# Optimization experiments

Measured on AMD Instinct MI355X. Metric: run time of the kernel, lower is better.

Reference implementation:

```python
import jax, jax.numpy as jnp
import numpy as np

N_HEADS = 32
N_KV_HEADS = 8
HEAD_DIM = 64
ROPE_THETA = 10000.0
NEG_INF = -1e9


def apply_rope(t, offset=0):
    # t: [B, H, L, hd]; half-split (rotate-half) RoPE convention
    B, H, L, hd = t.shape
    pos = jnp.arange(offset, offset + L, dtype=jnp.float32)            # [L]
    inv_freq = 1.0 / (ROPE_THETA ** (jnp.arange(0, hd, 2, dtype=jnp.float32) / hd))  # [hd/2]
    ang = pos[:, None] * inv_freq[None, :]                              # [L, hd/2]
    cos = jnp.cos(ang).astype(t.dtype)
    sin = jnp.sin(ang).astype(t.dtype)
    t1, t2 = jnp.split(t, 2, axis=-1)                                   # each [B,H,L,hd/2]
    return jnp.concatenate([t1 * cos - t2 * sin, t1 * sin + t2 * cos], axis=-1)


def setup_inputs() -> dict:
    key = jax.random.key(0)
    ks = jax.random.split(key, 6)
    B, L, D = 1, 2048, 2048
    x = jax.random.normal(ks[0], (B, L, D), dtype=jnp.float32)
    attn_scale = jnp.ones((1,), dtype=jnp.float32)
    # causal additive mask: 0 on/below diagonal, -1e9 above
    mask = jnp.where(jnp.tril(jnp.ones((L, L), dtype=bool)), 0.0, NEG_INF).astype(jnp.float32)
    s = 0.02
    Wq = jax.random.normal(ks[1], (N_HEADS * HEAD_DIM, D), dtype=jnp.float32) * s
    Wk = jax.random.normal(ks[2], (N_KV_HEADS * HEAD_DIM, D), dtype=jnp.float32) * s
    Wv = jax.random.normal(ks[3], (N_KV_HEADS * HEAD_DIM, D), dtype=jnp.float32) * s
    Wo = jax.random.normal(ks[4], (D, N_HEADS * HEAD_DIM), dtype=jnp.float32) * s
    return {"x": x, "attn_scale": attn_scale, "mask": mask,
            "Wq": Wq, "Wk": Wk, "Wv": Wv, "Wo": Wo}


def reference(x, attn_scale, mask, Wq, Wk, Wv, Wo):
    B, L, D = x.shape
    scale = HEAD_DIM ** -0.5
    # projections (nn.Linear: y = x @ W.T)
    q = (x @ Wq.T).reshape(B, L, N_HEADS, HEAD_DIM).transpose(0, 2, 1, 3)     # [B,H,L,hd]
    k = (x @ Wk.T).reshape(B, L, N_KV_HEADS, HEAD_DIM).transpose(0, 2, 1, 3)  # [B,Hk,L,hd]
    v = (x @ Wv.T).reshape(B, L, N_KV_HEADS, HEAD_DIM).transpose(0, 2, 1, 3)
    q = apply_rope(q)
    k = apply_rope(k)
    q = q * attn_scale  # elementwise attn_scale applied to queries
    # GQA: repeat kv heads
    rep = N_HEADS // N_KV_HEADS
    k = jnp.repeat(k, rep, axis=1)
    v = jnp.repeat(v, rep, axis=1)
    scores = jnp.einsum('bhld,bhmd->bhlm', q, k) * scale + mask
    probs = jax.nn.softmax(scores, axis=-1)
    out = jnp.einsum('bhlm,bhmd->bhld', probs, v)          # [B,H,L,hd]
    out = out.transpose(0, 2, 1, 3).reshape(B, L, N_HEADS * HEAD_DIM)
    return out @ Wo.T
```

## Files before the change

kernel.cpp:

```cpp
#include <hip/hip_runtime.h>
#include <stdint.h>

typedef short bf16x8 __attribute__((ext_vector_type(8)));
typedef float f32x4 __attribute__((ext_vector_type(4)));

__device__ __forceinline__ unsigned short f2bf(float f) {
  uint32_t u = __float_as_uint(f);
  u = (u + 0x7FFFu + ((u >> 16) & 1u)) >> 16;
  return (unsigned short)u;
}
__device__ __forceinline__ float bf2f(unsigned short h) {
  return __uint_as_float(((uint32_t)h) << 16);
}

__device__ __forceinline__ void gload16(const void* g, void* lds) {
  const __attribute__((address_space(1))) char* gp =
      (const __attribute__((address_space(1))) char*)(uintptr_t)g;
  __attribute__((address_space(3))) char* sp =
      (__attribute__((address_space(3))) char*)(uint32_t)(uintptr_t)lds;
  __builtin_amdgcn_global_load_lds(gp, sp, 16, 0, 0);
}

__global__ void k_cvt_all(const float* __restrict__ x, const float* __restrict__ Wq,
                          const float* __restrict__ Wk, const float* __restrict__ Wv,
                          const float* __restrict__ Wo, unsigned short* __restrict__ xb,
                          unsigned short* __restrict__ Wcat, unsigned short* __restrict__ Wob) {
  int b = blockIdx.x;
  const float* src;
  unsigned short* dst;
  int off;
  if (b < 4096)       { src = x;  dst = xb;                  off = b; }
  else if (b < 8192)  { src = Wq; dst = Wcat;                off = b - 4096; }
  else if (b < 9216)  { src = Wk; dst = Wcat + 2048 * 2048;  off = b - 8192; }
  else if (b < 10240) { src = Wv; dst = Wcat + 2560 * 2048;  off = b - 9216; }
  else                { src = Wo; dst = Wob;                  off = b - 10240; }
  int i = off * 256 + threadIdx.x;
  float4 v = ((const float4*)src)[i];
  ushort4 o;
  o.x = f2bf(v.x); o.y = f2bf(v.y); o.z = f2bf(v.z); o.w = f2bf(v.w);
  ((ushort4*)dst)[i] = o;
}

template <int OUTF32>
__global__ __launch_bounds__(256) void k_gemm(const unsigned short* __restrict__ A,
                                              const unsigned short* __restrict__ B,
                                              void* __restrict__ Cout,
                                              int M, int N, int K) {
  __shared__ unsigned short As[128 * 64];
  __shared__ unsigned short Bs[128 * 64];
  const int tid = threadIdx.x;
  const int w = tid >> 6, lane = tid & 63;
  const int g = lane >> 4, cl = lane & 15;
  const int nTn = N >> 7;
  const int per = gridDim.x >> 3;
  const int bid = (blockIdx.x & 7) * per + (blockIdx.x >> 3);
  const int tm = bid / nTn, tn = bid % nTn;
  const int m0 = tm << 7, n0 = tn << 7;
  const int wm = (w >> 1) << 6, wn = (w & 1) << 6;
  f32x4 acc[4][4] = {};
  for (int kt = 0; kt < K; kt += 64) {
    if (kt) __syncthreads();
#pragma unroll
    for (int it = 0; it < 8; ++it) {
      int cc = tid + it * 256;
      int half = cc >> 10;
      int c3 = cc & 1023;
      int row = c3 >> 3, kb = (c3 & 7) << 4;
      const unsigned short* base = half ? (B + (size_t)(n0 + row) * K + kt)
                                        : (A + (size_t)(m0 + row) * K + kt);
      const char* src = (const char*)base + (kb ^ ((row & 7) << 4));
      char* dstl = (char*)(half ? Bs : As) + c3 * 16;
      gload16(src, dstl);
    }
    asm volatile("s_waitcnt vmcnt(0)" ::: "memory");
    __syncthreads();
#pragma unroll
    for (int ks = 0; ks < 2; ++ks) {
      bf16x8 af[4], bfr[4];
#pragma unroll
      for (int i = 0; i < 4; ++i) {
        int row = wm + i * 16 + cl;
        int kb = ((g << 4) + (ks << 6)) ^ ((row & 7) << 4);
        af[i] = *(const bf16x8*)((const char*)As + row * 128 + kb);
      }
#pragma unroll
      for (int j = 0; j < 4; ++j) {
        int row = wn + j * 16 + cl;
        int kb = ((g << 4) + (ks << 6)) ^ ((row & 7) << 4);
        bfr[j] = *(const bf16x8*)((const char*)Bs + row * 128 + kb);
      }
#pragma unroll
      for (int i = 0; i < 4; ++i)
#pragma unroll
        for (int j = 0; j < 4; ++j)
          acc[i][j] = __builtin_amdgcn_mfma_f32_16x16x32_bf16(af[i], bfr[j], acc[i][j], 0, 0, 0);
    }
  }
#pragma unroll
  for (int i = 0; i < 4; ++i)
#pragma unroll
    for (int j = 0; j < 4; ++j)
#pragma unroll
      for (int r = 0; r < 4; ++r) {
        int row = m0 + wm + i * 16 + (g << 2) + r;
        int col = n0 + wn + j * 16 + cl;
        float v = acc[i][j][r];
        if (OUTF32)
          ((float*)Cout)[(size_t)row * N + col] = v;
        else
          ((unsigned short*)Cout)[(size_t)row * N + col] = f2bf(v);
      }
}

__global__ void k_ropevt(unsigned short* __restrict__ qkv, const float* __restrict__ scale_p,
                         unsigned short* __restrict__ vt) {
  __shared__ unsigned short tl[64][80];
  if (blockIdx.x < 2560) {
    int idx = blockIdx.x * 256 + threadIdx.x;
    int l = idx / 320;
    int u = idx - l * 320;
    int h = u >> 3;
    int i4 = (u & 7) << 2;
    int colbase = (h < 32) ? (h << 6) : (2048 + ((h - 32) << 6));
    unsigned short* p = qkv + (size_t)l * 3072 + colbase + i4;
    float sc = (h < 32) ? (scale_p[0] * 0.125f * 1.4426950408889634f) : 1.0f;
    ushort4 a = *(const ushort4*)p;
    ushort4 b = *(const ushort4*)(p + 32);
    unsigned short av[4] = {a.x, a.y, a.z, a.w};
    unsigned short bv[4] = {b.x, b.y, b.z, b.w};
    unsigned short r1[4], r2[4];
#pragma unroll
    for (int j = 0; j < 4; ++j) {
      int i = i4 + j;
      float invf = __expf(-(float)i * 0.2878231366242557f);
      float ang = (float)l * invf;
      float cs = cosf(ang), sn = sinf(ang);
      float x1 = bf2f(av[j]), x2 = bf2f(bv[j]);
      r1[j] = f2bf((x1 * cs - x2 * sn) * sc);
      r2[j] = f2bf((x1 * sn + x2 * cs) * sc);
    }
    ushort4 oa = {r1[0], r1[1], r1[2], r1[3]};
    ushort4 ob = {r2[0], r2[1], r2[2], r2[3]};
    *(ushort4*)p = oa;
    *(ushort4*)(p + 32) = ob;
  } else {
    const int tid = threadIdx.x;
    const int bb = blockIdx.x - 2560;
    const int hk = bb >> 5, lt = bb & 31;
    const int l0 = lt << 6;
#pragma unroll
    for (int it = 0; it < 2; ++it) {
      int cc = tid + it * 256;
      int lr = cc >> 3, d0 = (cc & 7) << 3;
      uint4 v = *(const uint4*)(qkv + (size_t)(l0 + lr) * 3072 + 2560 + hk * 64 + d0);
      *(uint4*)&tl[lr][d0] = v;
    }
    __syncthreads();
#pragma unroll
    for (int it = 0; it < 2; ++it) {
      int cc = tid + it * 256;
      int dr = cc >> 3, le = (cc & 7) << 3;
      unsigned short tmp[8] __attribute__((aligned(16)));
#pragma unroll
      for (int j = 0; j < 8; ++j) tmp[j] = tl[le + j][dr];
      *(uint4*)(vt + (size_t)(hk * 64 + dr) * 2048 + l0 + le) = *(const uint4*)tmp;
    }
  }
}

__global__ __launch_bounds__(256) void k_attn(const unsigned short* __restrict__ qkv,
                                              const unsigned short* __restrict__ vt,
                                              unsigned short* __restrict__ ao) {
  __shared__ unsigned short Ks[2][64 * 64];
  __shared__ unsigned short Vs[3][64 * 64];
  __shared__ unsigned short Ps[4 * 16 * 64];
  const int tid = threadIdx.x;
  const int w = tid >> 6, lane = tid & 63;
  const int g = lane >> 4, cl = lane & 15;
  const int h = blockIdx.x & 31;
  const int qb = 31 - (blockIdx.x >> 5);
  const int q0 = qb << 6;
  const int hk = h >> 2;
  const int qg = q0 + w * 16 + cl;

  const unsigned short* qptr = qkv + (size_t)qg * 3072 + h * 64 + g * 8;
  bf16x8 qf0 = *(const bf16x8*)qptr;
  bf16x8 qf1 = *(const bf16x8*)(qptr + 32);

  float m_run = -3e38f, l_run = 0.0f;
  f32x4 acc[4] = {};

  const unsigned short* kbase = qkv + 2048 + hk * 64;
  const unsigned short* vbase = vt + (size_t)hk * 64 * 2048;
  char* myP = (char*)Ps + w * 2048;

  auto stageK = [&](int ck, int b) {
    const int kv0 = ck << 6;
#pragma unroll
    for (int it = 0; it < 2; ++it) {
      int cc = tid + it * 256;
      int row = cc >> 3, kb = (cc & 7) << 4;
      const char* src = (const char*)(kbase + (size_t)(kv0 + row) * 3072) + (kb ^ ((row & 7) << 4));
      gload16(src, (char*)Ks[b] + cc * 16);
    }
  };
  auto stageV = [&](int ck, int b) {
    const int kv0 = ck << 6;
#pragma unroll
    for (int it = 0; it < 2; ++it) {
      int cc = tid + it * 256;
      int row = cc >> 3, kb = (cc & 7) << 4;
      const char* src = (const char*)(vbase + (size_t)row * 2048 + kv0) + (kb ^ ((row & 7) << 4));
      gload16(src, (char*)Vs[b] + cc * 16);
    }
  };

  stageK(0, 0); stageV(0, 0);
  if (qb >= 1) { stageK(1, 1); stageV(1, 1); }
  asm volatile("s_waitcnt vmcnt(0)" ::: "memory");
  __syncthreads();

  float svP[4][4];
  {
    const char* Kc = (const char*)Ks[0];
    __builtin_amdgcn_s_setprio(1);
#pragma unroll
    for (int t = 0; t < 4; ++t) {
      f32x4 st = {};
#pragma unroll
      for (int ks = 0; ks < 2; ++ks) {
        int row = t * 16 + cl;
        int kb = ((g << 4) + (ks << 6)) ^ ((row & 7) << 4);
        bf16x8 kf = *(const bf16x8*)(Kc + row * 128 + kb);
        st = __builtin_amdgcn_mfma_f32_16x16x32_bf16(kf, ks ? qf1 : qf0, st, 0, 0, 0);
      }
#pragma unroll
      for (int r = 0; r < 4; ++r) svP[t][r] = st[r];
    }
    __builtin_amdgcn_s_setprio(0);
  }
  __syncthreads();

  for (int i = 0; i <= qb; ++i) {
    if (i + 2 <= qb) { stageK(i + 2, (i + 2) & 1); stageV(i + 2, (i + 2) % 3); }

    float svN[4][4];
    if (i < qb) {
      const char* Kc = (const char*)Ks[(i + 1) & 1];
      __builtin_amdgcn_s_setprio(1);
#pragma unroll
      for (int t = 0; t < 4; ++t) {
        f32x4 st = {};
#pragma unroll
        for (int ks = 0; ks < 2; ++ks) {
          int row = t * 16 + cl;
          int kb = ((g << 4) + (ks << 6)) ^ ((row & 7) << 4);
          bf16x8 kf = *(const bf16x8*)(Kc + row * 128 + kb);
          st = __builtin_amdgcn_mfma_f32_16x16x32_bf16(kf, ks ? qf1 : qf0, st, 0, 0, 0);
        }
#pragma unroll
        for (int r = 0; r < 4; ++r) svN[t][r] = st[r];
      }
      __builtin_amdgcn_s_setprio(0);
    }

    if (i == qb) {
      const int kv0 = i << 6;
#pragma unroll
      for (int t = 0; t < 4; ++t)
#pragma unroll
        for (int r = 0; r < 4; ++r) {
          int kvg = kv0 + t * 16 + (g << 2) + r;
          if (kvg > qg) svP[t][r] = -1e9f;
        }
    }
    float pmax = -3e38f;
#pragma unroll
    for (int t = 0; t < 4; ++t)
      pmax = fmaxf(pmax, fmaxf(fmaxf(svP[t][0], svP[t][1]), fmaxf(svP[t][2], svP[t][3])));
    pmax = fmaxf(pmax, __shfl_xor(pmax, 16));
    pmax = fmaxf(pmax, __shfl_xor(pmax, 32));
    if (!__all(pmax - m_run <= 8.0f)) {
      float m_new = fmaxf(m_run, pmax);
      float fac = __builtin_exp2f(m_run - m_new);
      float fr[4];
#pragma unroll
      for (int r = 0; r < 4; ++r) fr[r] = __shfl(fac, (g << 2) + r);
#pragma unroll
      for (int t = 0; t < 4; ++t) {
        acc[t][0] *= fr[0]; acc[t][1] *= fr[1]; acc[t][2] *= fr[2]; acc[t][3] *= fr[3];
      }
      l_run *= fac;
      m_run = m_new;
    }
    float psum = 0.0f;
#pragma unroll
    for (int t = 0; t < 4; ++t) {
      float e0 = __builtin_exp2f(svP[t][0] - m_run);
      float e1 = __builtin_exp2f(svP[t][1] - m_run);
      float e2 = __builtin_exp2f(svP[t][2] - m_run);
      float e3 = __builtin_exp2f(svP[t][3] - m_run);
      psum += (e0 + e1) + (e2 + e3);
      uint32_t d0, d1;
      asm("v_cvt_pk_bf16_f32 %0, %1, %2" : "=v"(d0) : "v"(e0), "v"(e1));
      asm("v_cvt_pk_bf16_f32 %0, %1, %2" : "=v"(d1) : "v"(e2), "v"(e3));
      uint2 dd; dd.x = d0; dd.y = d1;
      int kb = ((t << 5) + (g << 3)) ^ ((cl & 7) << 4);
      *(uint2*)(myP + cl * 128 + kb) = dd;
    }
    psum += __shfl_xor(psum, 16);
    psum += __shfl_xor(psum, 32);
    l_run += psum;

    {
      const char* Vc = (const char*)Vs[i % 3];
      __builtin_amdgcn_s_setprio(1);
#pragma unroll
      for (int ks = 0; ks < 2; ++ks) {
        int kbp = ((g << 4) + (ks << 6)) ^ ((cl & 7) << 4);
        bf16x8 pf = *(const bf16x8*)(myP + cl * 128 + kbp);
#pragma unroll
        for (int t = 0; t < 4; ++t) {
          int row = t * 16 + cl;
          int kbv = ((g << 4) + (ks << 6)) ^ ((row & 7) << 4);
          bf16x8 vf = *(const bf16x8*)(Vc + row * 128 + kbv);
          acc[t] = __builtin_amdgcn_mfma_f32_16x16x32_bf16(pf, vf, acc[t], 0, 0, 0);
        }
      }
      __builtin_amdgcn_s_setprio(0);
    }

    if (i < qb) {
      asm volatile("s_waitcnt vmcnt(0)" ::: "memory");
      __syncthreads();
#pragma unroll
      for (int t = 0; t < 4; ++t)
#pragma unroll
        for (int r = 0; r < 4; ++r) svP[t][r] = svN[t][r];
    }
  }

  float li[4];
#pragma unroll
  for (int r = 0; r < 4; ++r) li[r] = 1.0f / __shfl(l_run, (g << 2) + r);
#pragma unroll
  for (int t = 0; t < 4; ++t)
#pragma unroll
    for (int r = 0; r < 4; ++r) {
      int row = q0 + w * 16 + (g << 2) + r;
      int col = h * 64 + t * 16 + cl;
      ao[(size_t)row * 2048 + col] = f2bf(acc[t][r] * li[r]);
    }
}

extern "C" void kernel_launch(void* const* d_in, const int* in_sizes, int n_in,
                              void* d_out, int out_size, void* d_ws, size_t ws_size,
                              hipStream_t stream) {
  (void)in_sizes; (void)n_in; (void)out_size; (void)ws_size;
  const float* x  = (const float*)d_in[0];
  const float* sc = (const float*)d_in[1];
  const float* Wq = (const float*)d_in[3];
  const float* Wk = (const float*)d_in[4];
  const float* Wv = (const float*)d_in[5];
  const float* Wo = (const float*)d_in[6];
  float* out = (float*)d_out;
  char* ws = (char*)d_ws;
  unsigned short* xb   = (unsigned short*)(ws);
  unsigned short* Wcat = (unsigned short*)(ws + 8388608);
  unsigned short* Wob  = (unsigned short*)(ws + 20971520);
  unsigned short* QKV  = (unsigned short*)(ws + 29360128);
  unsigned short* VT   = (unsigned short*)(ws + 41943040);
  unsigned short* AO   = (unsigned short*)(ws + 44040192);

  k_cvt_all<<<14336, 256, 0, stream>>>(x, Wq, Wk, Wv, Wo, xb, Wcat, Wob);
  k_gemm<0><<<384, 256, 0, stream>>>(xb, Wcat, QKV, 2048, 3072, 2048);
  k_ropevt<<<2816, 256, 0, stream>>>(QKV, sc, VT);
  k_attn<<<1024, 256, 0, stream>>>(QKV, VT, AO);
  k_gemm<1><<<256, 256, 0, stream>>>(AO, Wob, out, 2048, 2048, 2048);
}
```

Baseline: 141.3 us.

## Double-buffer GEMM LDS tiles and loosen attention prefetch waits

```diff
diff --git a/kernel.cpp b/kernel.cpp
--- a/kernel.cpp
+++ b/kernel.cpp
@@ -46,8 +46,8 @@
                                               const unsigned short* __restrict__ B,
                                               void* __restrict__ Cout,
                                               int M, int N, int K) {
-  __shared__ unsigned short As[128 * 64];
-  __shared__ unsigned short Bs[128 * 64];
+  __shared__ unsigned short As[2][128 * 64];
+  __shared__ unsigned short Bs[2][128 * 64];
   const int tid = threadIdx.x;
   const int w = tid >> 6, lane = tid & 63;
   const int g = lane >> 4, cl = lane & 15;
@@ -58,8 +58,8 @@
   const int m0 = tm << 7, n0 = tn << 7;
   const int wm = (w >> 1) << 6, wn = (w & 1) << 6;
   f32x4 acc[4][4] = {};
-  for (int kt = 0; kt < K; kt += 64) {
-    if (kt) __syncthreads();
+
+  auto stage = [&](int kt, int b) {
 #pragma unroll
     for (int it = 0; it < 8; ++it) {
       int cc = tid + it * 256;
@@ -69,11 +69,18 @@
       const unsigned short* base = half ? (B + (size_t)(n0 + row) * K + kt)
                                         : (A + (size_t)(m0 + row) * K + kt);
       const char* src = (const char*)base + (kb ^ ((row & 7) << 4));
-      char* dstl = (char*)(half ? Bs : As) + c3 * 16;
+      char* dstl = (char*)(half ? Bs[b] : As[b]) + c3 * 16;
       gload16(src, dstl);
     }
-    asm volatile("s_waitcnt vmcnt(0)" ::: "memory");
-    __syncthreads();
+  };
+
+  stage(0, 0);
+  asm volatile("s_waitcnt vmcnt(0)" ::: "memory");
+  __syncthreads();
+  int buf = 0;
+
+  for (int kt = 0; kt < K; kt += 64) {
+    if (kt + 64 < K) stage(kt + 64, buf ^ 1);
 #pragma unroll
     for (int ks = 0; ks < 2; ++ks) {
       bf16x8 af[4], bfr[4];
@@ -81,13 +88,13 @@
       for (int i = 0; i < 4; ++i) {
         int row = wm + i * 16 + cl;
         int kb = ((g << 4) + (ks << 6)) ^ ((row & 7) << 4);
-        af[i] = *(const bf16x8*)((const char*)As + row * 128 + kb);
+        af[i] = *(const bf16x8*)((const char*)As[buf] + row * 128 + kb);
       }
 #pragma unroll
       for (int j = 0; j < 4; ++j) {
         int row = wn + j * 16 + cl;
         int kb = ((g << 4) + (ks << 6)) ^ ((row & 7) << 4);
-        bfr[j] = *(const bf16x8*)((const char*)Bs + row * 128 + kb);
+        bfr[j] = *(const bf16x8*)((const char*)Bs[buf] + row * 128 + kb);
       }
 #pragma unroll
       for (int i = 0; i < 4; ++i)
@@ -95,6 +102,9 @@
         for (int j = 0; j < 4; ++j)
           acc[i][j] = __builtin_amdgcn_mfma_f32_16x16x32_bf16(af[i], bfr[j], acc[i][j], 0, 0, 0);
     }
+    asm volatile("s_waitcnt vmcnt(0)" ::: "memory");
+    __syncthreads();
+    buf ^= 1;
   }
 #pragma unroll
   for (int i = 0; i < 4; ++i)
@@ -242,7 +252,8 @@
   __syncthreads();
 
   for (int i = 0; i <= qb; ++i) {
-    if (i + 2 <= qb) { stageK(i + 2, (i + 2) & 1); stageV(i + 2, (i + 2) % 3); }
+    const bool deep = (i + 2 <= qb);
+    if (deep) stageK(i + 2, (i + 2) & 1);
 
     float svN[4][4];
     if (i < qb) {
@@ -264,6 +275,8 @@
       __builtin_amdgcn_s_setprio(0);
     }
 
+    if (deep) stageV(i + 2, (i + 2) % 3);
+
     if (i == qb) {
       const int kv0 = i << 6;
 #pragma unroll
@@ -274,10 +287,11 @@
           if (kvg > qg) svP[t][r] = -1e9f;
         }
     }
-    float pmax = -3e38f;
+    float pm[4];
 #pragma unroll
     for (int t = 0; t < 4; ++t)
-      pmax = fmaxf(pmax, fmaxf(fmaxf(svP[t][0], svP[t][1]), fmaxf(svP[t][2], svP[t][3])));
+      pm[t] = fmaxf(fmaxf(svP[t][0], svP[t][1]), fmaxf(svP[t][2], svP[t][3]));
+    float pmax = fmaxf(fmaxf(pm[0], pm[1]), fmaxf(pm[2], pm[3]));
     pmax = fmaxf(pmax, __shfl_xor(pmax, 16));
     pmax = fmaxf(pmax, __shfl_xor(pmax, 32));
     if (!__all(pmax - m_run <= 8.0f)) {
@@ -293,14 +307,14 @@
       l_run *= fac;
       m_run = m_new;
     }
-    float psum = 0.0f;
+    float ps[4];
 #pragma unroll
     for (int t = 0; t < 4; ++t) {
       float e0 = __builtin_exp2f(svP[t][0] - m_run);
       float e1 = __builtin_exp2f(svP[t][1] - m_run);
       float e2 = __builtin_exp2f(svP[t][2] - m_run);
       float e3 = __builtin_exp2f(svP[t][3] - m_run);
-      psum += (e0 + e1) + (e2 + e3);
+      ps[t] = (e0 + e1) + (e2 + e3);
       uint32_t d0, d1;
       asm("v_cvt_pk_bf16_f32 %0, %1, %2" : "=v"(d0) : "v"(e0), "v"(e1));
       asm("v_cvt_pk_bf16_f32 %0, %1, %2" : "=v"(d1) : "v"(e2), "v"(e3));
@@ -308,6 +322,7 @@
       int kb = ((t << 5) + (g << 3)) ^ ((cl & 7) << 4);
       *(uint2*)(myP + cl * 128 + kb) = dd;
     }
+    float psum = (ps[0] + ps[1]) + (ps[2] + ps[3]);
     psum += __shfl_xor(psum, 16);
     psum += __shfl_xor(psum, 32);
     l_run += psum;
@@ -331,7 +346,10 @@
     }
 
     if (i < qb) {
-      asm volatile("s_waitcnt vmcnt(0)" ::: "memory");
+      if (deep)
+        asm volatile("s_waitcnt vmcnt(2)" ::: "memory");
+      else
+        asm volatile("s_waitcnt vmcnt(0)" ::: "memory");
       __syncthreads();
 #pragma unroll
       for (int t = 0; t < 4; ++t)
```

After: 128.9 us. 1.1x faster.
